# Performance work log

Hardware: AMD Instinct MI355X
Metric: run time of the kernel (lower is better)

Reference implementation:

```python
import jax, jax.numpy as jnp
import numpy as np

B, D, N = 8, 1024, 1024
INTER, H = 512, 16
EPS = 1e-5


def conv1x1(x, W, b):
    # x: (B, Cin, N), W: (Cout, Cin), b: (Cout,) -> (B, Cout, N)
    return jnp.einsum('oc,bcn->bon', W, x) + b[None, :, None]


def setup_inputs() -> dict:
    key = jax.random.key(0)
    ks = jax.random.split(key, 12)
    s = 0.02
    v = jax.random.normal(ks[0], (B, D, N), jnp.float32)
    mask = (jax.random.uniform(ks[1], (B, N)) < 0.9).astype(jnp.float32)
    Wg = jax.random.normal(ks[2], (INTER, D), jnp.float32) * s
    bg = jax.random.normal(ks[3], (INTER,), jnp.float32) * s
    Wt = jax.random.normal(ks[4], (INTER, D), jnp.float32) * s
    bt = jax.random.normal(ks[5], (INTER,), jnp.float32) * s
    Wp = jax.random.normal(ks[6], (INTER, D), jnp.float32) * s
    bp = jax.random.normal(ks[7], (INTER,), jnp.float32) * s
    Ww = jax.random.normal(ks[8], (D, INTER), jnp.float32) * s
    bw = jax.random.normal(ks[9], (D,), jnp.float32) * s
    bn_gamma = jax.random.normal(ks[10], (D,), jnp.float32) * s + 1.0
    bn_beta = jax.random.normal(ks[11], (D,), jnp.float32) * s
    bn_mean = jnp.zeros((D,), jnp.float32)
    bn_var = jnp.ones((D,), jnp.float32)
    return {"v": v, "mask": mask, "Wg": Wg, "bg": bg, "Wt": Wt, "bt": bt,
            "Wp": Wp, "bp": bp, "Ww": Ww, "bw": bw, "bn_gamma": bn_gamma,
            "bn_beta": bn_beta, "bn_mean": bn_mean, "bn_var": bn_var}


def reference(v, mask, Wg, bg, Wt, bt, Wp, bp, Ww, bw,
              bn_gamma, bn_beta, bn_mean, bn_var):
    b, d, n = v.shape
    hd = INTER // H  # head dim
    # projections (1x1 conv == per-node linear); move to (B, N, INTER)
    g_v = conv1x1(v, Wg, bg).transpose(0, 2, 1) * mask[:, :, None]
    theta = conv1x1(v, Wt, bt).transpose(0, 2, 1)
    phi = conv1x1(v, Wp, bp).transpose(0, 2, 1)
    theta4 = theta.reshape(b, n, H, hd)  # (B, N, H, hd)
    phi4 = phi.reshape(b, n, H, hd)
    g4 = g_v.reshape(b, n, H, hd)
    # relation matrix R: (B, H, N, N)
    R = jnp.einsum('bnhd,bmhd->bhnm', theta4, phi4)
    C = jnp.sum(mask, axis=1)  # (B,)
    Rm = (R / C[:, None, None, None]) * mask[:, None, :, None] * mask[:, None, None, :]
    # aggregate: (B, N, H, hd)
    y = jnp.einsum('bhnm,bmhd->bnhd', Rm, g4).reshape(b, n, INTER)
    y = y.transpose(0, 2, 1)  # (B, INTER, N)
    # output projection + BatchNorm1d (eval form) + residual
    Wy = conv1x1(y, Ww, bw)
    inv = bn_gamma / jnp.sqrt(bn_var + EPS)
    Wy = (Wy - bn_mean[None, :, None]) * inv[None, :, None] + bn_beta[None, :, None]
    Wy = Wy * mask[:, None, :]
    return Wy + v
```

## Files before the change

### kernel.cpp

```cpp
#include <hip/hip_runtime.h>
#include <hip/hip_bf16.h>
#include <stdint.h>

#define B_ 8
#define D_ 1024
#define N_ 1024
#define INTER_ 512
#define H_ 16
#define EPS_ 1e-5f

typedef __attribute__((ext_vector_type(8))) short bf16x8;
typedef __attribute__((ext_vector_type(4))) float f32x4;
typedef __attribute__((ext_vector_type(4))) unsigned short u16x4;

__device__ __forceinline__ unsigned short f2bf(float f) {
  union { float f; uint32_t u; } v; v.f = f;
  uint32_t r = (v.u + 0x7FFFu + ((v.u >> 16) & 1u)) >> 16;
  return (unsigned short)r;
}

__device__ __forceinline__ void gload_lds16(const void* g, void* l) {
  __builtin_amdgcn_global_load_lds(
      (const __attribute__((address_space(1))) void*)g,
      (__attribute__((address_space(3))) void*)l, 16, 0, 0);
}

__global__ void k_transpose(const float* __restrict__ v,
                            unsigned short* __restrict__ vT) {
  __shared__ float t[32][33];
  const int b = blockIdx.z;
  const int n0 = blockIdx.x * 32, d0 = blockIdx.y * 32;
  const int tx = threadIdx.x, ty = threadIdx.y;
  const float* src = v + ((size_t)b * D_ + d0) * N_ + n0;
#pragma unroll
  for (int i = 0; i < 4; ++i) t[ty + 8 * i][tx] = src[(ty + 8 * i) * N_ + tx];
  __syncthreads();
  unsigned short* dst = vT + ((size_t)b * N_ + n0) * D_ + d0;
#pragma unroll
  for (int i = 0; i < 4; ++i) dst[(ty + 8 * i) * D_ + tx] = f2bf(t[tx][ty + 8 * i]);
}

__global__ void k_cast_w(const float* __restrict__ Wt, const float* __restrict__ Wp,
                         const float* __restrict__ Wg, const float* __restrict__ Ww,
                         unsigned short* __restrict__ Wall,
                         unsigned short* __restrict__ Wwb) {
  const int idx4 = blockIdx.x * 256 + threadIdx.x;
  const int total1 = 1536 * 1024 / 4;
  if (idx4 < total1) {
    const int idx = idx4 * 4;
    const int row = idx >> 10, c = idx & 1023;
    const float* src = row < 512    ? Wt + row * 1024 + c
                       : row < 1024 ? Wp + (row - 512) * 1024 + c
                                    : Wg + (row - 1024) * 1024 + c;
    float4 f = *(const float4*)src;
    u16x4 o = {f2bf(f.x), f2bf(f.y), f2bf(f.z), f2bf(f.w)};
    *(u16x4*)(Wall + idx) = o;
  } else {
    const int idx = (idx4 - total1) * 4;
    float4 f = *(const float4*)(Ww + idx);
    u16x4 o = {f2bf(f.x), f2bf(f.y), f2bf(f.z), f2bf(f.w)};
    *(u16x4*)(Wwb + idx) = o;
  }
}

__global__ void k_prep_small(const float* __restrict__ bt, const float* __restrict__ bp,
                             const float* __restrict__ bg, const float* __restrict__ mask,
                             float* __restrict__ ball, float* __restrict__ invC) {
  if (blockIdx.x == 0) {
    for (int i = threadIdx.x; i < 512; i += 256) {
      ball[i] = bt[i]; ball[512 + i] = bp[i]; ball[1024 + i] = bg[i];
    }
  } else {
    const int b = blockIdx.x - 1;
    float s = 0.f;
    for (int i = threadIdx.x; i < 1024; i += 256) s += mask[b * 1024 + i];
    for (int off = 32; off; off >>= 1) s += __shfl_down(s, off, 64);
    __shared__ float red[4];
    if ((threadIdx.x & 63) == 0) red[threadIdx.x >> 6] = s;
    __syncthreads();
    if (threadIdx.x == 0) invC[b] = 1.0f / (red[0] + red[1] + red[2] + red[3]);
  }
}

#define BM 128
#define BN 128
#define BK 64

__global__ __launch_bounds__(256, 2) void k_gemm1(
    const unsigned short* __restrict__ Wall, const unsigned short* __restrict__ vT,
    const float* __restrict__ ball, const float* __restrict__ mask,
    unsigned short* __restrict__ thT, unsigned short* __restrict__ phi,
    unsigned short* __restrict__ g) {
  __shared__ __align__(16) unsigned short lA[BM * BK];
  __shared__ __align__(16) unsigned short lB[BN * BK];
  const int b = blockIdx.z, bx = blockIdx.x, by = blockIdx.y;
  const int tid = threadIdx.x, lane = tid & 63, w = tid >> 6;
  const int wr = w >> 1, wc = w & 1;

  const unsigned short* Abase = Wall + (size_t)(by * BM) * 1024;
  const unsigned short* Bbase = vT + ((size_t)b * N_ + bx * BN) * 1024;

  const int srow = w * 32 + (lane >> 3);
  const int sgl = lane & 7;

  f32x4 acc[4][4] = {};

  for (int kt = 0; kt < 1024 / BK; ++kt) {
#pragma unroll
    for (int i = 0; i < 4; ++i) {
      const int r = srow + i * 8;
      const int gs = sgl ^ (r & 7);
      gload_lds16(Abase + (size_t)r * 1024 + kt * BK + gs * 8,
                  (char*)lA + w * 4096 + i * 1024);
      gload_lds16(Bbase + (size_t)r * 1024 + kt * BK + gs * 8,
                  (char*)lB + w * 4096 + i * 1024);
    }
    __syncthreads();
#pragma unroll
    for (int kk = 0; kk < 2; ++kk) {
      bf16x8 af[4], bfr[4];
#pragma unroll
      for (int mf = 0; mf < 4; ++mf) {
        const int r = wr * 64 + mf * 16 + (lane & 15);
        int byte = r * 128 + kk * 64 + ((lane >> 4) * 16);
        byte ^= (r & 7) << 4;
        af[mf] = *(const bf16x8*)((const char*)lA + byte);
      }
#pragma unroll
      for (int nf = 0; nf < 4; ++nf) {
        const int r = wc * 64 + nf * 16 + (lane & 15);
        int byte = r * 128 + kk * 64 + ((lane >> 4) * 16);
        byte ^= (r & 7) << 4;
        bfr[nf] = *(const bf16x8*)((const char*)lB + byte);
      }
#pragma unroll
      for (int mf = 0; mf < 4; ++mf)
#pragma unroll
        for (int nf = 0; nf < 4; ++nf)
          acc[mf][nf] = __builtin_amdgcn_mfma_f32_16x16x32_bf16(
              af[mf], bfr[nf], acc[mf][nf], 0, 0, 0);
    }
    __syncthreads();
  }

  const int region = by >> 2;
#pragma unroll
  for (int mf = 0; mf < 4; ++mf) {
#pragma unroll
    for (int nf = 0; nf < 4; ++nf) {
      const int col = bx * BN + wc * 64 + nf * 16 + (lane & 15);
      const int row0 = by * BM + wr * 64 + mf * 16 + ((lane >> 4) << 2);
      if (region == 0) {
        u16x4 o;
#pragma unroll
        for (int r = 0; r < 4; ++r) o[r] = f2bf(acc[mf][nf][r] + ball[row0 + r]);
        *(u16x4*)(thT + ((size_t)b * N_ + col) * 512 + row0) = o;
      } else if (region == 1) {
#pragma unroll
        for (int r = 0; r < 4; ++r)
          phi[((size_t)b * 512 + (row0 + r - 512)) * 1024 + col] =
              f2bf(acc[mf][nf][r] + ball[row0 + r]);
      } else {
        const float mv = mask[b * 1024 + col];
#pragma unroll
        for (int r = 0; r < 4; ++r)
          g[((size_t)b * 512 + (row0 + r - 1024)) * 1024 + col] =
              f2bf((acc[mf][nf][r] + ball[row0 + r]) * mv);
      }
    }
  }
}

__global__ __launch_bounds__(256) void k_S(const unsigned short* __restrict__ phi,
                                           const unsigned short* __restrict__ g,
                                           unsigned short* __restrict__ S) {
  const int bh = blockIdx.x, b = bh >> 4, h = bh & 15;
  const int tid = threadIdx.x, lane = tid & 63, w = tid >> 6;
  const unsigned short* pb = phi + ((size_t)b * 512 + h * 32) * 1024;
  const unsigned short* gb = g + ((size_t)b * 512 + h * 32) * 1024;
  f32x4 acc[2][2] = {};
  for (int it = 0; it < 8; ++it) {
    const int n = w * 256 + it * 32 + ((lane >> 4) * 8);
    bf16x8 af[2], bfr[2];
#pragma unroll
    for (int mf = 0; mf < 2; ++mf)
      af[mf] = *(const bf16x8*)(pb + (size_t)(mf * 16 + (lane & 15)) * 1024 + n);
#pragma unroll
    for (int nf = 0; nf < 2; ++nf)
      bfr[nf] = *(const bf16x8*)(gb + (size_t)(nf * 16 + (lane & 15)) * 1024 + n);
#pragma unroll
    for (int mf = 0; mf < 2; ++mf)
#pragma unroll
      for (int nf = 0; nf < 2; ++nf)
        acc[mf][nf] = __builtin_amdgcn_mfma_f32_16x16x32_bf16(
            af[mf], bfr[nf], acc[mf][nf], 0, 0, 0);
  }
  __shared__ float red[4][32][32];
#pragma unroll
  for (int mf = 0; mf < 2; ++mf)
#pragma unroll
    for (int nf = 0; nf < 2; ++nf)
#pragma unroll
      for (int r = 0; r < 4; ++r)
        red[w][mf * 16 + (lane >> 4) * 4 + r][nf * 16 + (lane & 15)] = acc[mf][nf][r];
  __syncthreads();
  for (int e = tid; e < 1024; e += 256) {
    const int r = e >> 5, c = e & 31;
    S[(size_t)bh * 1024 + e] =
        f2bf(red[0][r][c] + red[1][r][c] + red[2][r][c] + red[3][r][c]);
  }
}

__global__ __launch_bounds__(256) void k_M(const unsigned short* __restrict__ Wwb,
                                           const unsigned short* __restrict__ S,
                                           unsigned short* __restrict__ M) {
  const int rb = blockIdx.x, h = blockIdx.y, b = blockIdx.z;
  const int tid = threadIdx.x, lane = tid & 63, w = tid >> 6;
  const int row0w = rb * 128 + w * 32;
  const unsigned short* Sb = S + (size_t)(b * 16 + h) * 1024;
  f32x4 acc[2][2] = {};
  bf16x8 af[2], bfr[2];
#pragma unroll
  for (int mf = 0; mf < 2; ++mf)
    af[mf] = *(const bf16x8*)(Wwb + (size_t)(row0w + mf * 16 + (lane & 15)) * 512 +
                              h * 32 + (lane >> 4) * 8);
#pragma unroll
  for (int nf = 0; nf < 2; ++nf)
    bfr[nf] = *(const bf16x8*)(Sb + (size_t)(nf * 16 + (lane & 15)) * 32 +
                               (lane >> 4) * 8);
#pragma unroll
  for (int mf = 0; mf < 2; ++mf)
#pragma unroll
    for (int nf = 0; nf < 2; ++nf)
      acc[mf][nf] = __builtin_amdgcn_mfma_f32_16x16x32_bf16(
          af[mf], bfr[nf], acc[mf][nf], 0, 0, 0);
#pragma unroll
  for (int mf = 0; mf < 2; ++mf)
#pragma unroll
    for (int nf = 0; nf < 2; ++nf)
#pragma unroll
      for (int r = 0; r < 4; ++r) {
        const int row = row0w + mf * 16 + (lane >> 4) * 4 + r;
        const int dp = nf * 16 + (lane & 15);
        M[((size_t)b * 1024 + row) * 512 + h * 32 + dp] = f2bf(acc[mf][nf][r]);
      }
}

__global__ __launch_bounds__(256, 2) void k_gemm2(
    const unsigned short* __restrict__ M, const unsigned short* __restrict__ thT,
    const float* __restrict__ mask, const float* __restrict__ invC,
    const float* __restrict__ bw, const float* __restrict__ gamma,
    const float* __restrict__ beta, const float* __restrict__ mean,
    const float* __restrict__ var, const float* __restrict__ vin,
    float* __restrict__ out) {
  __shared__ __align__(16) unsigned short lA[BM * BK];
  __shared__ __align__(16) unsigned short lB[BN * BK];
  const int b = blockIdx.z, bx = blockIdx.x, by = blockIdx.y;
  const int tid = threadIdx.x, lane = tid & 63, w = tid >> 6;
  const int wr = w >> 1, wc = w & 1;

  const unsigned short* Abase = M + ((size_t)b * 1024 + by * BM) * 512;
  const unsigned short* Bbase = thT + ((size_t)b * N_ + bx * BN) * 512;

  const int srow = w * 32 + (lane >> 3);
  const int sgl = lane & 7;

  f32x4 acc[4][4] = {};

  for (int kt = 0; kt < 512 / BK; ++kt) {
#pragma unroll
    for (int i = 0; i < 4; ++i) {
      const int r = srow + i * 8;
      const int gs = sgl ^ (r & 7);
      gload_lds16(Abase + (size_t)r * 512 + kt * BK + gs * 8,
                  (char*)lA + w * 4096 + i * 1024);
      gload_lds16(Bbase + (size_t)r * 512 + kt * BK + gs * 8,
                  (char*)lB + w * 4096 + i * 1024);
    }
    __syncthreads();
#pragma unroll
    for (int kk = 0; kk < 2; ++kk) {
      bf16x8 af[4], bfr[4];
#pragma unroll
      for (int mf = 0; mf < 4; ++mf) {
        const int r = wr * 64 + mf * 16 + (lane & 15);
        int byte = r * 128 + kk * 64 + ((lane >> 4) * 16);
        byte ^= (r & 7) << 4;
        af[mf] = *(const bf16x8*)((const char*)lA + byte);
      }
#pragma unroll
      for (int nf = 0; nf < 4; ++nf) {
        const int r = wc * 64 + nf * 16 + (lane & 15);
        int byte = r * 128 + kk * 64 + ((lane >> 4) * 16);
        byte ^= (r & 7) << 4;
        bfr[nf] = *(const bf16x8*)((const char*)lB + byte);
      }
#pragma unroll
      for (int mf = 0; mf < 4; ++mf)
#pragma unroll
        for (int nf = 0; nf < 4; ++nf)
          acc[mf][nf] = __builtin_amdgcn_mfma_f32_16x16x32_bf16(
              af[mf], bfr[nf], acc[mf][nf], 0, 0, 0);
    }
    __syncthreads();
  }

  const float icb = invC[b];
#pragma unroll
  for (int mf = 0; mf < 4; ++mf) {
#pragma unroll
    for (int nf = 0; nf < 4; ++nf) {
      const int col = bx * BN + wc * 64 + nf * 16 + (lane & 15);
      const int row0 = by * BM + wr * 64 + mf * 16 + ((lane >> 4) << 2);
      const float mv = mask[b * 1024 + col];
      const float sc = mv * icb;
#pragma unroll
      for (int r = 0; r < 4; ++r) {
        const int o = row0 + r;
        float val = acc[mf][nf][r] * sc + bw[o];
        const float inv = gamma[o] * rsqrtf(var[o] + EPS_);
        val = (val - mean[o]) * inv + beta[o];
        const size_t idx = ((size_t)b * 1024 + o) * 1024 + col;
        out[idx] = val * mv + vin[idx];
      }
    }
  }
}

extern "C" void kernel_launch(void* const* d_in, const int* in_sizes, int n_in,
                              void* d_out, int out_size, void* d_ws, size_t ws_size,
                              hipStream_t stream) {
  const float* v = (const float*)d_in[0];
  const float* mask = (const float*)d_in[1];
  const float* Wg = (const float*)d_in[2];
  const float* bg = (const float*)d_in[3];
  const float* Wt = (const float*)d_in[4];
  const float* bt = (const float*)d_in[5];
  const float* Wp = (const float*)d_in[6];
  const float* bp = (const float*)d_in[7];
  const float* Ww = (const float*)d_in[8];
  const float* bw = (const float*)d_in[9];
  const float* gamma = (const float*)d_in[10];
  const float* beta = (const float*)d_in[11];
  const float* mean = (const float*)d_in[12];
  const float* var = (const float*)d_in[13];
  float* out = (float*)d_out;

  char* ws = (char*)d_ws;
  unsigned short* vT = (unsigned short*)ws;    ws += 16777216;
  unsigned short* Wall = (unsigned short*)ws;  ws += 3145728;
  unsigned short* Wwb = (unsigned short*)ws;   ws += 1048576;
  unsigned short* thT = (unsigned short*)ws;   ws += 8388608;
  unsigned short* phi = (unsigned short*)ws;   ws += 8388608;
  unsigned short* g = (unsigned short*)ws;     ws += 8388608;
  unsigned short* S = (unsigned short*)ws;     ws += 262144;
  unsigned short* Mw = (unsigned short*)ws;    ws += 8388608;
  float* ball = (float*)ws;                    ws += 6144;
  float* invC = (float*)ws;                    ws += 32;

  k_transpose<<<dim3(32, 32, 8), dim3(32, 8), 0, stream>>>(v, vT);
  k_cast_w<<<2048, 256, 0, stream>>>(Wt, Wp, Wg, Ww, Wall, Wwb);
  k_prep_small<<<9, 256, 0, stream>>>(bt, bp, bg, mask, ball, invC);
  k_gemm1<<<dim3(8, 12, 8), 256, 0, stream>>>(Wall, vT, ball, mask, thT, phi, g);
  k_S<<<128, 256, 0, stream>>>(phi, g, S);
  k_M<<<dim3(8, 16, 8), 256, 0, stream>>>(Wwb, S, Mw);
  k_gemm2<<<dim3(8, 8, 8), 256, 0, stream>>>(Mw, thT, mask, invC, bw, gamma, beta,
                                             mean, var, v, out);
}
```

Measured before the change: 175.3 us.

## Fuse prep kernels, stage GEMM1 epilogue via LDS, split S reduction across blocks

The three preprocessing kernels are merged into one launch. The transpose now uses 64x64 tiles with float4 reads and 16-byte bf16 writes. The GEMM1 epilogue stages outputs through LDS so that stores to thT, phi and g become coalesced 16-byte writes. The phi·g reduction is split into 8 sequence chunks across 1024 blocks instead of 128 (k_S becomes k_Spart), writing fp32 partials that k_M sums before its MFMA. This exposes more parallelism and cuts launch overhead, at the cost of extra partial-sum traffic and larger LDS use in GEMM1.

After: 176.5 us. About the same (+0.7%).

```diff
diff --git a/kernel.cpp b/kernel.cpp
--- a/kernel.cpp
+++ b/kernel.cpp
@@ -12,6 +12,7 @@
 typedef __attribute__((ext_vector_type(8))) short bf16x8;
 typedef __attribute__((ext_vector_type(4))) float f32x4;
 typedef __attribute__((ext_vector_type(4))) unsigned short u16x4;
+typedef __attribute__((ext_vector_type(8))) unsigned short u16x8;
 
 __device__ __forceinline__ unsigned short f2bf(float f) {
   union { float f; uint32_t u; } v; v.f = f;
@@ -25,60 +26,71 @@
       (__attribute__((address_space(3))) void*)l, 16, 0, 0);
 }
 
-__global__ void k_transpose(const float* __restrict__ v,
-                            unsigned short* __restrict__ vT) {
-  __shared__ float t[32][33];
-  const int b = blockIdx.z;
-  const int n0 = blockIdx.x * 32, d0 = blockIdx.y * 32;
-  const int tx = threadIdx.x, ty = threadIdx.y;
-  const float* src = v + ((size_t)b * D_ + d0) * N_ + n0;
-#pragma unroll
-  for (int i = 0; i < 4; ++i) t[ty + 8 * i][tx] = src[(ty + 8 * i) * N_ + tx];
-  __syncthreads();
-  unsigned short* dst = vT + ((size_t)b * N_ + n0) * D_ + d0;
-#pragma unroll
-  for (int i = 0; i < 4; ++i) dst[(ty + 8 * i) * D_ + tx] = f2bf(t[tx][ty + 8 * i]);
-}
-
-__global__ void k_cast_w(const float* __restrict__ Wt, const float* __restrict__ Wp,
-                         const float* __restrict__ Wg, const float* __restrict__ Ww,
-                         unsigned short* __restrict__ Wall,
-                         unsigned short* __restrict__ Wwb) {
-  const int idx4 = blockIdx.x * 256 + threadIdx.x;
-  const int total1 = 1536 * 1024 / 4;
-  if (idx4 < total1) {
-    const int idx = idx4 * 4;
-    const int row = idx >> 10, c = idx & 1023;
-    const float* src = row < 512    ? Wt + row * 1024 + c
-                       : row < 1024 ? Wp + (row - 512) * 1024 + c
-                                    : Wg + (row - 1024) * 1024 + c;
-    float4 f = *(const float4*)src;
-    u16x4 o = {f2bf(f.x), f2bf(f.y), f2bf(f.z), f2bf(f.w)};
-    *(u16x4*)(Wall + idx) = o;
+__global__ __launch_bounds__(256) void k_prep(
+    const float* __restrict__ v, const float* __restrict__ Wt,
+    const float* __restrict__ Wp, const float* __restrict__ Wg,
+    const float* __restrict__ Ww, const float* __restrict__ bt,
+    const float* __restrict__ bp, const float* __restrict__ bg,
+    const float* __restrict__ mask, unsigned short* __restrict__ vT,
+    unsigned short* __restrict__ Wall, unsigned short* __restrict__ Wwb,
+    float* __restrict__ ball, float* __restrict__ invC) {
+  const int blk = blockIdx.x, tid = threadIdx.x;
+  if (blk < 2048) {
+    __shared__ short T[64 * 72];
+    const int b = blk >> 8, tile = blk & 255;
+    const int n0 = (tile & 15) * 64, d0 = (tile >> 4) * 64;
+    const float* src = v + ((size_t)b * D_ + d0) * N_ + n0;
+    const int c = tid & 15, rg = tid >> 4;
+#pragma unroll
+    for (int i = 0; i < 4; ++i) {
+      const int r = rg * 4 + i;
+      float4 f = *(const float4*)(src + (size_t)r * N_ + c * 4);
+      const int nl = c * 4;
+      T[(nl + 0) * 72 + r] = f2bf(f.x);
+      T[(nl + 1) * 72 + r] = f2bf(f.y);
+      T[(nl + 2) * 72 + r] = f2bf(f.z);
+      T[(nl + 3) * 72 + r] = f2bf(f.w);
+    }
+    __syncthreads();
+    unsigned short* dst = vT + ((size_t)b * N_ + n0) * D_ + d0;
+    const int ch = tid & 7, nr = tid >> 3;
+#pragma unroll
+    for (int jj = 0; jj < 2; ++jj) {
+      const int nl = nr + jj * 32;
+      u16x8 val = *(const u16x8*)&T[nl * 72 + ch * 8];
+      *(u16x8*)(dst + (size_t)nl * D_ + ch * 8) = val;
+    }
+  } else if (blk < 4096) {
+    const int idx4 = (blk - 2048) * 256 + tid;
+    const int total1 = 1536 * 1024 / 4;
+    if (idx4 < total1) {
+      const int idx = idx4 * 4;
+      const int row = idx >> 10, c = idx & 1023;
+      const float* src = row < 512    ? Wt + row * 1024 + c
+                         : row < 1024 ? Wp + (row - 512) * 1024 + c
+                                      : Wg + (row - 1024) * 1024 + c;
+      float4 f = *(const float4*)src;
+      u16x4 o = {f2bf(f.x), f2bf(f.y), f2bf(f.z), f2bf(f.w)};
+      *(u16x4*)(Wall + idx) = o;
+    } else {
+      const int idx = (idx4 - total1) * 4;
+      float4 f = *(const float4*)(Ww + idx);
+      u16x4 o = {f2bf(f.x), f2bf(f.y), f2bf(f.z), f2bf(f.w)};
+      *(u16x4*)(Wwb + idx) = o;
+    }
+  } else if (blk == 4096) {
+    for (int i = tid; i < 512; i += 256) {
+      ball[i] = bt[i]; ball[512 + i] = bp[i]; ball[1024 + i] = bg[i];
+    }
   } else {
-    const int idx = (idx4 - total1) * 4;
-    float4 f = *(const float4*)(Ww + idx);
-    u16x4 o = {f2bf(f.x), f2bf(f.y), f2bf(f.z), f2bf(f.w)};
-    *(u16x4*)(Wwb + idx) = o;
-  }
-}
-
-__global__ void k_prep_small(const float* __restrict__ bt, const float* __restrict__ bp,
-                             const float* __restrict__ bg, const float* __restrict__ mask,
-                             float* __restrict__ ball, float* __restrict__ invC) {
-  if (blockIdx.x == 0) {
-    for (int i = threadIdx.x; i < 512; i += 256) {
-      ball[i] = bt[i]; ball[512 + i] = bp[i]; ball[1024 + i] = bg[i];
-    }
-  } else {
-    const int b = blockIdx.x - 1;
+    const int b = blk - 4097;
     float s = 0.f;
-    for (int i = threadIdx.x; i < 1024; i += 256) s += mask[b * 1024 + i];
+    for (int i = tid; i < 1024; i += 256) s += mask[b * 1024 + i];
     for (int off = 32; off; off >>= 1) s += __shfl_down(s, off, 64);
     __shared__ float red[4];
-    if ((threadIdx.x & 63) == 0) red[threadIdx.x >> 6] = s;
-    __syncthreads();
-    if (threadIdx.x == 0) invC[b] = 1.0f / (red[0] + red[1] + red[2] + red[3]);
+    if ((tid & 63) == 0) red[tid >> 6] = s;
+    __syncthreads();
+    if (tid == 0) invC[b] = 1.0f / (red[0] + red[1] + red[2] + red[3]);
   }
 }
 
@@ -91,8 +103,9 @@
     const float* __restrict__ ball, const float* __restrict__ mask,
     unsigned short* __restrict__ thT, unsigned short* __restrict__ phi,
     unsigned short* __restrict__ g) {
-  __shared__ __align__(16) unsigned short lA[BM * BK];
-  __shared__ __align__(16) unsigned short lB[BN * BK];
+  __shared__ __align__(16) short smem[128 * 132];
+  char* lA = (char*)smem;
+  char* lB = lA + 16384;
   const int b = blockIdx.z, bx = blockIdx.x, by = blockIdx.y;
   const int tid = threadIdx.x, lane = tid & 63, w = tid >> 6;
   const int wr = w >> 1, wc = w & 1;
@@ -111,9 +124,9 @@
       const int r = srow + i * 8;
       const int gs = sgl ^ (r & 7);
       gload_lds16(Abase + (size_t)r * 1024 + kt * BK + gs * 8,
-                  (char*)lA + w * 4096 + i * 1024);
+                  lA + w * 4096 + i * 1024);
       gload_lds16(Bbase + (size_t)r * 1024 + kt * BK + gs * 8,
-                  (char*)lB + w * 4096 + i * 1024);
+                  lB + w * 4096 + i * 1024);
     }
     __syncthreads();
 #pragma unroll
@@ -124,14 +137,14 @@
         const int r = wr * 64 + mf * 16 + (lane & 15);
         int byte = r * 128 + kk * 64 + ((lane >> 4) * 16);
         byte ^= (r & 7) << 4;
-        af[mf] = *(const bf16x8*)((const char*)lA + byte);
+        af[mf] = *(const bf16x8*)(lA + byte);
       }
 #pragma unroll
       for (int nf = 0; nf < 4; ++nf) {
         const int r = wc * 64 + nf * 16 + (lane & 15);
         int byte = r * 128 + kk * 64 + ((lane >> 4) * 16);
         byte ^= (r & 7) << 4;
-        bfr[nf] = *(const bf16x8*)((const char*)lB + byte);
+        bfr[nf] = *(const bf16x8*)(lB + byte);
       }
 #pragma unroll
       for (int mf = 0; mf < 4; ++mf)
@@ -144,57 +157,75 @@
   }
 
   const int region = by >> 2;
-#pragma unroll
-  for (int mf = 0; mf < 4; ++mf) {
-#pragma unroll
-    for (int nf = 0; nf < 4; ++nf) {
-      const int col = bx * BN + wc * 64 + nf * 16 + (lane & 15);
-      const int row0 = by * BM + wr * 64 + mf * 16 + ((lane >> 4) << 2);
-      if (region == 0) {
+  short* Tc = smem;
+  if (region == 0) {
+#pragma unroll
+    for (int mf = 0; mf < 4; ++mf)
+#pragma unroll
+      for (int nf = 0; nf < 4; ++nf) {
+        const int nl = wc * 64 + nf * 16 + (lane & 15);
+        const int ol0 = wr * 64 + mf * 16 + ((lane >> 4) << 2);
         u16x4 o;
 #pragma unroll
-        for (int r = 0; r < 4; ++r) o[r] = f2bf(acc[mf][nf][r] + ball[row0 + r]);
-        *(u16x4*)(thT + ((size_t)b * N_ + col) * 512 + row0) = o;
-      } else if (region == 1) {
-#pragma unroll
         for (int r = 0; r < 4; ++r)
-          phi[((size_t)b * 512 + (row0 + r - 512)) * 1024 + col] =
-              f2bf(acc[mf][nf][r] + ball[row0 + r]);
-      } else {
-        const float mv = mask[b * 1024 + col];
+          o[r] = f2bf(acc[mf][nf][r] + ball[by * BM + ol0 + r]);
+        *(u16x4*)&Tc[nl * 132 + ol0] = o;
+      }
+  } else {
+#pragma unroll
+    for (int mf = 0; mf < 4; ++mf)
+#pragma unroll
+      for (int nf = 0; nf < 4; ++nf) {
+        const int nl = wc * 64 + nf * 16 + (lane & 15);
+        const int ol0 = wr * 64 + mf * 16 + ((lane >> 4) << 2);
+        const float mv = (region == 2) ? mask[b * 1024 + bx * BN + nl] : 1.0f;
 #pragma unroll
         for (int r = 0; r < 4; ++r)
-          g[((size_t)b * 512 + (row0 + r - 1024)) * 1024 + col] =
-              f2bf((acc[mf][nf][r] + ball[row0 + r]) * mv);
-      }
-    }
-  }
-}
-
-__global__ __launch_bounds__(256) void k_S(const unsigned short* __restrict__ phi,
-                                           const unsigned short* __restrict__ g,
-                                           unsigned short* __restrict__ S) {
-  const int bh = blockIdx.x, b = bh >> 4, h = bh & 15;
+          Tc[(ol0 + r) * 132 + nl] =
+              f2bf((acc[mf][nf][r] + ball[by * BM + ol0 + r]) * mv);
+      }
+  }
+  __syncthreads();
+  const int ch = tid & 15;
+#pragma unroll
+  for (int j = 0; j < 8; ++j) {
+    const int row = (tid >> 4) + j * 16;
+    u16x4 lo = *(const u16x4*)&Tc[row * 132 + ch * 8];
+    u16x4 hi = *(const u16x4*)&Tc[row * 132 + ch * 8 + 4];
+    u16x8 val = {lo[0], lo[1], lo[2], lo[3], hi[0], hi[1], hi[2], hi[3]};
+    unsigned short* dst;
+    if (region == 0)
+      dst = thT + ((size_t)b * N_ + bx * BN + row) * 512 + by * BM + ch * 8;
+    else if (region == 1)
+      dst = phi + ((size_t)b * 512 + (by - 4) * BM + row) * 1024 + bx * BN + ch * 8;
+    else
+      dst = g + ((size_t)b * 512 + (by - 8) * BM + row) * 1024 + bx * BN + ch * 8;
+    *(u16x8*)dst = val;
+  }
+}
+
+__global__ __launch_bounds__(256) void k_Spart(const unsigned short* __restrict__ phi,
+                                               const unsigned short* __restrict__ g,
+                                               float* __restrict__ Spart) {
+  const int s = blockIdx.x, h = blockIdx.y, b = blockIdx.z;
   const int tid = threadIdx.x, lane = tid & 63, w = tid >> 6;
-  const unsigned short* pb = phi + ((size_t)b * 512 + h * 32) * 1024;
-  const unsigned short* gb = g + ((size_t)b * 512 + h * 32) * 1024;
+  const unsigned short* pb = phi + ((size_t)b * 512 + h * 32) * 1024 + s * 128;
+  const unsigned short* gb = g + ((size_t)b * 512 + h * 32) * 1024 + s * 128;
+  const int n = w * 32 + ((lane >> 4) * 8);
+  bf16x8 af[2], bfr[2];
+#pragma unroll
+  for (int mf = 0; mf < 2; ++mf)
+    af[mf] = *(const bf16x8*)(pb + (size_t)(mf * 16 + (lane & 15)) * 1024 + n);
+#pragma unroll
+  for (int nf = 0; nf < 2; ++nf)
+    bfr[nf] = *(const bf16x8*)(gb + (size_t)(nf * 16 + (lane & 15)) * 1024 + n);
   f32x4 acc[2][2] = {};
-  for (int it = 0; it < 8; ++it) {
-    const int n = w * 256 + it * 32 + ((lane >> 4) * 8);
-    bf16x8 af[2], bfr[2];
-#pragma unroll
-    for (int mf = 0; mf < 2; ++mf)
-      af[mf] = *(const bf16x8*)(pb + (size_t)(mf * 16 + (lane & 15)) * 1024 + n);
+#pragma unroll
+  for (int mf = 0; mf < 2; ++mf)
 #pragma unroll
     for (int nf = 0; nf < 2; ++nf)
-      bfr[nf] = *(const bf16x8*)(gb + (size_t)(nf * 16 + (lane & 15)) * 1024 + n);
-#pragma unroll
-    for (int mf = 0; mf < 2; ++mf)
-#pragma unroll
-      for (int nf = 0; nf < 2; ++nf)
-        acc[mf][nf] = __builtin_amdgcn_mfma_f32_16x16x32_bf16(
-            af[mf], bfr[nf], acc[mf][nf], 0, 0, 0);
-  }
+      acc[mf][nf] = __builtin_amdgcn_mfma_f32_16x16x32_bf16(
+          af[mf], bfr[nf], acc[mf][nf], 0, 0, 0);
   __shared__ float red[4][32][32];
 #pragma unroll
   for (int mf = 0; mf < 2; ++mf)
@@ -204,20 +235,38 @@
       for (int r = 0; r < 4; ++r)
         red[w][mf * 16 + (lane >> 4) * 4 + r][nf * 16 + (lane & 15)] = acc[mf][nf][r];
   __syncthreads();
-  for (int e = tid; e < 1024; e += 256) {
-    const int r = e >> 5, c = e & 31;
-    S[(size_t)bh * 1024 + e] =
-        f2bf(red[0][r][c] + red[1][r][c] + red[2][r][c] + red[3][r][c]);
-  }
+  float* dst = Spart + ((size_t)(b * 16 + h) * 8 + s) * 1024;
+  const int e0 = tid * 4;
+  float4 s0 = *(const float4*)(&red[0][0][0] + e0);
+  float4 s1 = *(const float4*)(&red[1][0][0] + e0);
+  float4 s2 = *(const float4*)(&red[2][0][0] + e0);
+  float4 s3 = *(const float4*)(&red[3][0][0] + e0);
+  float4 o = {s0.x + s1.x + s2.x + s3.x, s0.y + s1.y + s2.y + s3.y,
+              s0.z + s1.z + s2.z + s3.z, s0.w + s1.w + s2.w + s3.w};
+  *(float4*)(dst + e0) = o;
 }
 
 __global__ __launch_bounds__(256) void k_M(const unsigned short* __restrict__ Wwb,
-                                           const unsigned short* __restrict__ S,
+                                           const float* __restrict__ Spart,
                                            unsigned short* __restrict__ M) {
   const int rb = blockIdx.x, h = blockIdx.y, b = blockIdx.z;
   const int tid = threadIdx.x, lane = tid & 63, w = tid >> 6;
+  __shared__ short Sb[32 * 40];
+  {
+    const int e0 = tid * 4;
+    const float* sp = Spart + (size_t)(b * 16 + h) * 8 * 1024 + e0;
+    float4 a = {0, 0, 0, 0};
+#pragma unroll
+    for (int s = 0; s < 8; ++s) {
+      float4 p = *(const float4*)(sp + s * 1024);
+      a.x += p.x; a.y += p.y; a.z += p.z; a.w += p.w;
+    }
+    const int row = e0 >> 5, col = e0 & 31;
+    u16x4 sv = {f2bf(a.x), f2bf(a.y), f2bf(a.z), f2bf(a.w)};
+    *(u16x4*)&Sb[row * 40 + col] = sv;
+  }
+  __syncthreads();
   const int row0w = rb * 128 + w * 32;
-  const unsigned short* Sb = S + (size_t)(b * 16 + h) * 1024;
   f32x4 acc[2][2] = {};
   bf16x8 af[2], bfr[2];
 #pragma unroll
@@ -226,8 +275,7 @@
                               h * 32 + (lane >> 4) * 8);
 #pragma unroll
   for (int nf = 0; nf < 2; ++nf)
-    bfr[nf] = *(const bf16x8*)(Sb + (size_t)(nf * 16 + (lane & 15)) * 32 +
-                               (lane >> 4) * 8);
+    bfr[nf] = *(const bf16x8*)&Sb[(nf * 16 + (lane & 15)) * 40 + (lane >> 4) * 8];
 #pragma unroll
   for (int mf = 0; mf < 2; ++mf)
 #pragma unroll
@@ -353,17 +401,16 @@
   unsigned short* thT = (unsigned short*)ws;   ws += 8388608;
   unsigned short* phi = (unsigned short*)ws;   ws += 8388608;
   unsigned short* g = (unsigned short*)ws;     ws += 8388608;
-  unsigned short* S = (unsigned short*)ws;     ws += 262144;
+  float* Spart = (float*)ws;                   ws += 4194304;
   unsigned short* Mw = (unsigned short*)ws;    ws += 8388608;
   float* ball = (float*)ws;                    ws += 6144;
   float* invC = (float*)ws;                    ws += 32;
 
-  k_transpose<<<dim3(32, 32, 8), dim3(32, 8), 0, stream>>>(v, vT);
-  k_cast_w<<<2048, 256, 0, stream>>>(Wt, Wp, Wg, Ww, Wall, Wwb);
-  k_prep_small<<<9, 256, 0, stream>>>(bt, bp, bg, mask, ball, invC);
+  k_prep<<<4105, 256, 0, stream>>>(v, Wt, Wp, Wg, Ww, bt, bp, bg, mask,
+                                   vT, Wall, Wwb, ball, invC);
   k_gemm1<<<dim3(8, 12, 8), 256, 0, stream>>>(Wall, vT, ball, mask, thT, phi, g);
-  k_S<<<128, 256, 0, stream>>>(phi, g, S);
-  k_M<<<dim3(8, 16, 8), 256, 0, stream>>>(Wwb, S, Mw);
+  k_Spart<<<dim3(8, 16, 8), 256, 0, stream>>>(phi, g, Spart);
+  k_M<<<dim3(8, 16, 8), 256, 0, stream>>>(Wwb, Spart, Mw);
   k_gemm2<<<dim3(8, 8, 8), 256, 0, stream>>>(Mw, thT, mask, invC, bw, gamma, beta,
                                              mean, var, v, out);
 }
```
